# Kernel optimization log

Hardware: AMD Instinct MI355X
Metric: run time of the kernel (lower is better)

## Reference

```python
import jax, jax.numpy as jnp
import numpy as np

GAMMA = 0.00390625  # 1/256


def setup_inputs() -> dict:
    key = jax.random.key(0)
    ks = jax.random.split(key, 8)
    B, F, S = 65536, 256, 1024
    return {
        "x": jax.random.normal(ks[0], (B, F), dtype=jnp.float32),
        "sv": jax.random.normal(ks[1], (S, F), dtype=jnp.float32),
        "W1": jax.random.normal(ks[2], (S, S), dtype=jnp.float32) * (1.0 / np.sqrt(S)),
        "b1": jax.random.normal(ks[3], (S,), dtype=jnp.float32) * 0.01,
        "W2": jax.random.normal(ks[4], (S, S), dtype=jnp.float32) * (1.0 / np.sqrt(S)),
        "b2": jax.random.normal(ks[5], (S,), dtype=jnp.float32) * 0.01,
        "Wh": jax.random.normal(ks[6], (2, S), dtype=jnp.float32) * (1.0 / np.sqrt(S)),
        "bh": jax.random.normal(ks[7], (2,), dtype=jnp.float32) * 0.01,
    }


def reference(x, sv, W1, b1, W2, b2, Wh, bh):
    # RBF kernel features: k[b, s] = exp(-gamma * ||x_b - sv_s||^2)
    # Expand squared distance to avoid a (B, S, F) intermediate.
    x2 = jnp.sum(x * x, axis=-1, keepdims=True)          # (B, 1)
    s2 = jnp.sum(sv * sv, axis=-1)[None, :]              # (1, S)
    d2 = x2 + s2 - 2.0 * jnp.einsum("bf,sf->bs", x, sv)  # (B, S)
    k = jnp.exp(-GAMMA * d2)                              # (B, S)
    # MLP classifier: depth=2 hidden ReLU layers + 2-logit head
    h = jax.nn.relu(jnp.einsum("bs,os->bo", k, W1) + b1)
    h = jax.nn.relu(jnp.einsum("bs,os->bo", h, W2) + b2)
    return jnp.einsum("bs,os->bo", h, Wh) + bh           # (B, 2)
```

## Files before the change

kernel.cpp:

```cpp
#include <hip/hip_runtime.h>

typedef _Float16 f16x8 __attribute__((ext_vector_type(8)));
typedef _Float16 f16x4 __attribute__((ext_vector_type(4)));
typedef float    f32x4 __attribute__((ext_vector_type(4)));

#define GAMMA_F 0.00390625f

__global__ __launch_bounds__(256) void prep_rows_kernel(
    const float* __restrict__ src, _Float16* __restrict__ dst,
    float* __restrict__ sq, int nrows)
{
    int lane = threadIdx.x & 63, w = threadIdx.x >> 6;
    int row = blockIdx.x * 4 + w;
    if (row >= nrows) return;
    float4 v = ((const float4*)(src + (size_t)row * 256))[lane];
    f16x4 h;
    h[0] = (_Float16)v.x; h[1] = (_Float16)v.y;
    h[2] = (_Float16)v.z; h[3] = (_Float16)v.w;
    *((f16x4*)(dst + (size_t)row * 256) + lane) = h;
    float ss = v.x*v.x + v.y*v.y + v.z*v.z + v.w*v.w;
#pragma unroll
    for (int off = 32; off; off >>= 1) ss += __shfl_down(ss, off);
    if (lane == 0) sq[row] = ss;
}

__global__ __launch_bounds__(256) void cvt_kernel(
    const float* __restrict__ src, _Float16* __restrict__ dst, int n4)
{
    int i = blockIdx.x * 256 + threadIdx.x;
    if (i < n4) {
        float4 v = ((const float4*)src)[i];
        f16x4 h;
        h[0] = (_Float16)v.x; h[1] = (_Float16)v.y;
        h[2] = (_Float16)v.z; h[3] = (_Float16)v.w;
        ((f16x4*)dst)[i] = h;
    }
}

#define SBAR()  __builtin_amdgcn_s_barrier()
#define AS1 __attribute__((address_space(1)))
#define AS3 __attribute__((address_space(3)))

#define GLD(gptr, dstoff) __builtin_amdgcn_global_load_lds(                    \
    (const AS1 void*)(gptr), (AS3 void*)(ldsb + (dstoff)), 16, 0, 0)

#define STAGE_A(slot, half) do {                                               \
    GLD(aStage + (size_t)(half)*128*K,        (slot)*32768 + (half)*16384 + tb);          \
    GLD(aStage + (size_t)(half)*128*K + 64*K, (slot)*32768 + (half)*16384 + 8192 + tb);   \
} while (0)
#define STAGE_B(slot, half) do {                                               \
    GLD(bStage + (size_t)(half)*128*K,        65536 + (slot)*32768 + (half)*16384 + tb);        \
    GLD(bStage + (size_t)(half)*128*K + 64*K, 65536 + (slot)*32768 + (half)*16384 + 8192 + tb); \
} while (0)

#define READ_A(s, mh) do {                                                     \
    _Pragma("unroll") for (int mi = 0; mi < 4; ++mi) {                         \
        afr[0][mi] = *(const f16x8*)(ldsb + aO0 + (s)*32768 + (mh)*8192 + mi*2048); \
        afr[1][mi] = *(const f16x8*)(ldsb + aO1 + (s)*32768 + (mh)*8192 + mi*2048); \
    } } while (0)

#define READ_B(s, nh) do {                                                     \
    _Pragma("unroll") for (int nb = 0; nb < 2; ++nb) {                         \
        bfr[0][(nh)*2+nb] = *(const f16x8*)(ldsb + bO0 + (s)*32768 + (nh)*4096 + nb*2048); \
        bfr[1][(nh)*2+nb] = *(const f16x8*)(ldsb + bO1 + (s)*32768 + (nh)*4096 + nb*2048); \
    } } while (0)

#define MFMA16(mh, nh) do {                                                    \
    __builtin_amdgcn_s_setprio(1);                                             \
    _Pragma("unroll") for (int mi = 0; mi < 4; ++mi)                           \
    _Pragma("unroll") for (int nb = 0; nb < 2; ++nb)                           \
    _Pragma("unroll") for (int ks = 0; ks < 2; ++ks)                           \
        acc[(mh)*4+mi][(nh)*2+nb] = __builtin_amdgcn_mfma_f32_16x16x32_f16(    \
            afr[ks][mi], bfr[ks][(nh)*2+nb], acc[(mh)*4+mi][(nh)*2+nb], 0,0,0);\
    __builtin_amdgcn_s_setprio(0);                                             \
} while (0)

template <int MODE, int K>
__global__ __launch_bounds__(512, 1) void gemm256_kernel(
    const _Float16* __restrict__ A, const _Float16* __restrict__ B,
    _Float16* __restrict__ C, const float* __restrict__ e0,
    const float* __restrict__ e1)
{
    constexpr int KT = K / 64;
    constexpr int NITER = KT / 2;
    __shared__ f16x8 lds[8192];
    char* ldsb = (char*)lds;

    const int t    = threadIdx.x;
    const int tb   = t * 16;
    const int lane = t & 63, w = t >> 6;
    const int wr   = w >> 2, wc = w & 3;
    const int lrow = lane & 15, kq = lane >> 4;

    int bid  = blockIdx.x;
    int cpx  = (int)(gridDim.x >> 3);
    int lbid = (bid & 7) * cpx + (bid >> 3);
    int bm   = lbid >> 2, bn = lbid & 3;
    int rowA0 = bm * 256, rowB0 = bn * 256;

    const int aO0 = ((wr*128 + lrow)*8 + ( kq      ^ (lrow & 7))) * 16;
    const int aO1 = ((wr*128 + lrow)*8 + ((4 + kq) ^ (lrow & 7))) * 16;
    const int bO0 = 65536 + ((wc*64 + lrow)*8 + ( kq      ^ (lrow & 7))) * 16;
    const int bO1 = 65536 + ((wc*64 + lrow)*8 + ((4 + kq) ^ (lrow & 7))) * 16;

    const int prow = t >> 3;
    const int cg   = (t & 7) ^ (prow & 7);
    const _Float16* aStage = A + (size_t)(rowA0 + prow) * K + cg * 8;
    const _Float16* bStage = B + (size_t)(rowB0 + prow) * K + cg * 8;

    f32x4 acc[8][4];
#pragma unroll
    for (int i = 0; i < 8; ++i)
#pragma unroll
        for (int j = 0; j < 4; ++j) acc[i][j] = (f32x4){0.f, 0.f, 0.f, 0.f};

    f16x8 afr[2][4], bfr[2][4];

    STAGE_A(0, 0); STAGE_A(0, 1); STAGE_B(0, 0); STAGE_B(0, 1);
    aStage += 64; bStage += 64;
    STAGE_A(1, 0); STAGE_A(1, 1); STAGE_B(1, 0); STAGE_B(1, 1);
    aStage += 64; bStage += 64;
    asm volatile("s_waitcnt vmcnt(8)" ::: "memory");
    SBAR();

    for (int j = 0; j < NITER; ++j) {
        const bool last = (j == NITER - 1);

        READ_A(0, 0); READ_B(0, 0);
        if (j > 0) STAGE_A(1, 0);
        SBAR();
        MFMA16(0, 0);
        SBAR();
        READ_B(0, 1);
        if (j > 0) { STAGE_A(1, 1); aStage += 64; }
        SBAR();
        MFMA16(0, 1);
        SBAR();
        READ_A(0, 1);
        if (!last) STAGE_B(0, 0);
        SBAR();
        MFMA16(1, 0);
        SBAR();
        if (!last) {
            STAGE_B(0, 1); bStage += 64;
            asm volatile("s_waitcnt vmcnt(4)" ::: "memory");
        } else {
            asm volatile("s_waitcnt vmcnt(0)" ::: "memory");
        }
        SBAR();
        MFMA16(1, 1);
        SBAR();
        READ_A(1, 0); READ_B(1, 0);
        if (!last) STAGE_A(0, 0);
        SBAR();
        MFMA16(0, 0);
        SBAR();
        READ_B(1, 1);
        if (!last) { STAGE_A(0, 1); aStage += 64; }
        SBAR();
        MFMA16(0, 1);
        SBAR();
        READ_A(1, 1);
        if (!last) STAGE_B(1, 0);
        SBAR();
        MFMA16(1, 0);
        SBAR();
        if (!last) {
            STAGE_B(1, 1); bStage += 64;
            asm volatile("s_waitcnt vmcnt(4)" ::: "memory");
        }
        SBAR();
        MFMA16(1, 1);
        SBAR();
    }

    int gr0 = rowA0 + wr * 128;
    int gc0 = rowB0 + wc * 64;
    float ecol[4];
#pragma unroll
    for (int ni = 0; ni < 4; ++ni)
        ecol[ni] = (MODE == 0) ? e1[gc0 + ni * 16 + lrow]
                               : e0[gc0 + ni * 16 + lrow];
#pragma unroll
    for (int mi = 0; mi < 8; ++mi) {
#pragma unroll
        for (int jj = 0; jj < 4; ++jj) {
            int row = gr0 + mi * 16 + kq * 4 + jj;
            float xr = (MODE == 0) ? e0[row] : 0.f;
            size_t base = (size_t)row * 1024 + gc0 + lrow;
#pragma unroll
            for (int ni = 0; ni < 4; ++ni) {
                float v = acc[mi][ni][jj];
                if (MODE == 0) {
                    v = __expf(-GAMMA_F * (xr + ecol[ni] - 2.f * v));
                } else {
                    v += ecol[ni];
                    v = fmaxf(v, 0.f);
                }
                C[base + (size_t)ni * 16] = (_Float16)v;
            }
        }
    }
}

__global__ __launch_bounds__(256) void head_kernel(
    const _Float16* __restrict__ h2, const float* __restrict__ Wh,
    const float* __restrict__ bh, float* __restrict__ out)
{
    int lane = threadIdx.x & 63, w = threadIdx.x >> 6;
    int row = blockIdx.x * 4 + w;
    const _Float16* hp = h2 + (size_t)row * 1024;
    float s0 = 0.f, s1 = 0.f;
#pragma unroll
    for (int i = 0; i < 2; ++i) {
        int base = (i * 64 + lane) * 8;
        f16x8 hv = *(const f16x8*)(hp + base);
#pragma unroll
        for (int j = 0; j < 8; ++j) {
            float hj = (float)hv[j];
            s0 = fmaf(hj, Wh[base + j], s0);
            s1 = fmaf(hj, Wh[1024 + base + j], s1);
        }
    }
#pragma unroll
    for (int off = 32; off; off >>= 1) {
        s0 += __shfl_down(s0, off);
        s1 += __shfl_down(s1, off);
    }
    if (lane == 0) {
        out[(size_t)row * 2 + 0] = s0 + bh[0];
        out[(size_t)row * 2 + 1] = s1 + bh[1];
    }
}

extern "C" void kernel_launch(void* const* d_in, const int* in_sizes, int n_in,
                              void* d_out, int out_size, void* d_ws, size_t ws_size,
                              hipStream_t stream)
{
    const float* x  = (const float*)d_in[0];
    const float* sv = (const float*)d_in[1];
    const float* W1 = (const float*)d_in[2];
    const float* b1 = (const float*)d_in[3];
    const float* W2 = (const float*)d_in[4];
    const float* b2 = (const float*)d_in[5];
    const float* Wh = (const float*)d_in[6];
    const float* bh = (const float*)d_in[7];
    float* out = (float*)d_out;
    char* ws = (char*)d_ws;

    constexpr size_t OFF_SV = 0;
    constexpr size_t OFF_W1 = OFF_SV + 524288;
    constexpr size_t OFF_W2 = OFF_W1 + 2097152;
    constexpr size_t OFF_S2 = OFF_W2 + 2097152;
    constexpr size_t PERSIST = OFF_S2 + 4096;

    _Float16* svf = (_Float16*)(ws + OFF_SV);
    _Float16* w1f = (_Float16*)(ws + OFF_W1);
    _Float16* w2f = (_Float16*)(ws + OFF_W2);
    float*    s2v = (float*)(ws + OFF_S2);

    int Bc = 65536;
    while (Bc > 256 && PERSIST + (size_t)Bc * 4100ULL > ws_size) Bc >>= 1;

    char* chunk_base = ws + PERSIST;
    _Float16* kb  = (_Float16*)chunk_base;
    _Float16* h1b = (_Float16*)(chunk_base + (size_t)Bc * 2048);
    _Float16* xf  = h1b;
    float*    x2v = (float*)(chunk_base + (size_t)Bc * 4096);

    prep_rows_kernel<<<1024 / 4, 256, 0, stream>>>(sv, svf, s2v, 1024);
    cvt_kernel<<<1024, 256, 0, stream>>>(W1, w1f, 262144);
    cvt_kernel<<<1024, 256, 0, stream>>>(W2, w2f, 262144);

    int nchunks = 65536 / Bc;
    int ggrid   = (Bc / 256) * 4;
    for (int c = 0; c < nchunks; ++c) {
        const float* xc = x + (size_t)c * Bc * 256;
        prep_rows_kernel<<<Bc / 4, 256, 0, stream>>>(xc, xf, x2v, Bc);
        gemm256_kernel<0, 256><<<ggrid, 512, 0, stream>>>(xf, svf, kb, x2v, s2v);
        gemm256_kernel<1, 1024><<<ggrid, 512, 0, stream>>>(kb, w1f, h1b, b1, nullptr);
        gemm256_kernel<1, 1024><<<ggrid, 512, 0, stream>>>(h1b, w2f, kb, b2, nullptr);
        head_kernel<<<Bc / 4, 256, 0, stream>>>(kb, Wh, bh, out + (size_t)c * Bc * 2);
    }
}
```

Measured before the change: 398.0 us.

## Fuse output head into second hidden GEMM epilogue with atomics

The second hidden-layer GEMM now applies bias and ReLU and dots the result with both head weight rows in its epilogue. Partial sums are reduced across lanes and added to the output with atomics, which removes the separate head kernel and the f16 write and read of the second hidden activation. An init kernel seeds the output with the head bias. The MFMA loop order and LDS read/stage placement within the main loop are also reordered. In exchange, float atomic accumulation makes the output order-dependent and non-deterministic, and adds atomic traffic on a small output.

```diff
diff --git a/kernel.cpp b/kernel.cpp
--- a/kernel.cpp
+++ b/kernel.cpp
@@ -37,6 +37,13 @@
     }
 }
 
+__global__ __launch_bounds__(256) void init_out_kernel(
+    const float* __restrict__ bh, float* __restrict__ out, int n)
+{
+    int i = blockIdx.x * 256 + threadIdx.x;
+    if (i < n) ((float2*)out)[i] = make_float2(bh[0], bh[1]);
+}
+
 #define SBAR()  __builtin_amdgcn_s_barrier()
 #define AS1 __attribute__((address_space(1)))
 #define AS3 __attribute__((address_space(3)))
@@ -67,9 +74,9 @@
 
 #define MFMA16(mh, nh) do {                                                    \
     __builtin_amdgcn_s_setprio(1);                                             \
+    _Pragma("unroll") for (int ks = 0; ks < 2; ++ks)                           \
     _Pragma("unroll") for (int mi = 0; mi < 4; ++mi)                           \
     _Pragma("unroll") for (int nb = 0; nb < 2; ++nb)                           \
-    _Pragma("unroll") for (int ks = 0; ks < 2; ++ks)                           \
         acc[(mh)*4+mi][(nh)*2+nb] = __builtin_amdgcn_mfma_f32_16x16x32_f16(    \
             afr[ks][mi], bfr[ks][(nh)*2+nb], acc[(mh)*4+mi][(nh)*2+nb], 0,0,0);\
     __builtin_amdgcn_s_setprio(0);                                             \
@@ -79,7 +86,7 @@
 __global__ __launch_bounds__(512, 1) void gemm256_kernel(
     const _Float16* __restrict__ A, const _Float16* __restrict__ B,
     _Float16* __restrict__ C, const float* __restrict__ e0,
-    const float* __restrict__ e1)
+    const float* __restrict__ e1, float* __restrict__ outp)
 {
     constexpr int KT = K / 64;
     constexpr int NITER = KT / 2;
@@ -126,9 +133,10 @@
     for (int j = 0; j < NITER; ++j) {
         const bool last = (j == NITER - 1);
 
-        READ_A(0, 0); READ_B(0, 0);
+        READ_B(0, 0);
         if (j > 0) STAGE_A(1, 0);
         SBAR();
+        READ_A(0, 0);
         MFMA16(0, 0);
         SBAR();
         READ_B(0, 1);
@@ -136,9 +144,9 @@
         SBAR();
         MFMA16(0, 1);
         SBAR();
+        if (!last) STAGE_B(0, 0);
+        SBAR();
         READ_A(0, 1);
-        if (!last) STAGE_B(0, 0);
-        SBAR();
         MFMA16(1, 0);
         SBAR();
         if (!last) {
@@ -150,9 +158,10 @@
         SBAR();
         MFMA16(1, 1);
         SBAR();
-        READ_A(1, 0); READ_B(1, 0);
+        READ_B(1, 0);
         if (!last) STAGE_A(0, 0);
         SBAR();
+        READ_A(1, 0);
         MFMA16(0, 0);
         SBAR();
         READ_B(1, 1);
@@ -160,9 +169,9 @@
         SBAR();
         MFMA16(0, 1);
         SBAR();
+        if (!last) STAGE_B(1, 0);
+        SBAR();
         READ_A(1, 1);
-        if (!last) STAGE_B(1, 0);
-        SBAR();
         MFMA16(1, 0);
         SBAR();
         if (!last) {
@@ -181,6 +190,41 @@
     for (int ni = 0; ni < 4; ++ni)
         ecol[ni] = (MODE == 0) ? e1[gc0 + ni * 16 + lrow]
                                : e0[gc0 + ni * 16 + lrow];
+
+    if (MODE == 2) {
+        float wh0[4], wh1[4];
+#pragma unroll
+        for (int ni = 0; ni < 4; ++ni) {
+            int col = gc0 + ni * 16 + lrow;
+            wh0[ni] = e1[col];
+            wh1[ni] = e1[1024 + col];
+        }
+#pragma unroll
+        for (int mi = 0; mi < 8; ++mi) {
+#pragma unroll
+            for (int jj = 0; jj < 4; ++jj) {
+                int row = gr0 + mi * 16 + kq * 4 + jj;
+                float p0 = 0.f, p1 = 0.f;
+#pragma unroll
+                for (int ni = 0; ni < 4; ++ni) {
+                    float v = fmaxf(acc[mi][ni][jj] + ecol[ni], 0.f);
+                    p0 = fmaf(v, wh0[ni], p0);
+                    p1 = fmaf(v, wh1[ni], p1);
+                }
+#pragma unroll
+                for (int off = 1; off < 16; off <<= 1) {
+                    p0 += __shfl_xor(p0, off);
+                    p1 += __shfl_xor(p1, off);
+                }
+                if (lrow == 0) {
+                    atomicAdd(outp + (size_t)row * 2 + 0, p0);
+                    atomicAdd(outp + (size_t)row * 2 + 1, p1);
+                }
+            }
+        }
+        return;
+    }
+
 #pragma unroll
     for (int mi = 0; mi < 8; ++mi) {
 #pragma unroll
@@ -203,36 +247,6 @@
     }
 }
 
-__global__ __launch_bounds__(256) void head_kernel(
-    const _Float16* __restrict__ h2, const float* __restrict__ Wh,
-    const float* __restrict__ bh, float* __restrict__ out)
-{
-    int lane = threadIdx.x & 63, w = threadIdx.x >> 6;
-    int row = blockIdx.x * 4 + w;
-    const _Float16* hp = h2 + (size_t)row * 1024;
-    float s0 = 0.f, s1 = 0.f;
-#pragma unroll
-    for (int i = 0; i < 2; ++i) {
-        int base = (i * 64 + lane) * 8;
-        f16x8 hv = *(const f16x8*)(hp + base);
-#pragma unroll
-        for (int j = 0; j < 8; ++j) {
-            float hj = (float)hv[j];
-            s0 = fmaf(hj, Wh[base + j], s0);
-            s1 = fmaf(hj, Wh[1024 + base + j], s1);
-        }
-    }
-#pragma unroll
-    for (int off = 32; off; off >>= 1) {
-        s0 += __shfl_down(s0, off);
-        s1 += __shfl_down(s1, off);
-    }
-    if (lane == 0) {
-        out[(size_t)row * 2 + 0] = s0 + bh[0];
-        out[(size_t)row * 2 + 1] = s1 + bh[1];
-    }
-}
-
 extern "C" void kernel_launch(void* const* d_in, const int* in_sizes, int n_in,
                               void* d_out, int out_size, void* d_ws, size_t ws_size,
                               hipStream_t stream)
@@ -251,7 +265,8 @@
     constexpr size_t OFF_SV = 0;
     constexpr size_t OFF_W1 = OFF_SV + 524288;
     constexpr size_t OFF_W2 = OFF_W1 + 2097152;
-    constexpr size_t OFF_S2 = OFF_W2 + 2097152;
+    constexpr size_t OFF_WH = OFF_W2 + 2097152;
+    constexpr size_t OFF_S2 = OFF_WH + 8192;
     constexpr size_t PERSIST = OFF_S2 + 4096;
 
     _Float16* svf = (_Float16*)(ws + OFF_SV);
@@ -271,15 +286,16 @@
     prep_rows_kernel<<<1024 / 4, 256, 0, stream>>>(sv, svf, s2v, 1024);
     cvt_kernel<<<1024, 256, 0, stream>>>(W1, w1f, 262144);
     cvt_kernel<<<1024, 256, 0, stream>>>(W2, w2f, 262144);
+    init_out_kernel<<<256, 256, 0, stream>>>(bh, out, 65536);
 
     int nchunks = 65536 / Bc;
     int ggrid   = (Bc / 256) * 4;
     for (int c = 0; c < nchunks; ++c) {
         const float* xc = x + (size_t)c * Bc * 256;
         prep_rows_kernel<<<Bc / 4, 256, 0, stream>>>(xc, xf, x2v, Bc);
-        gemm256_kernel<0, 256><<<ggrid, 512, 0, stream>>>(xf, svf, kb, x2v, s2v);
-        gemm256_kernel<1, 1024><<<ggrid, 512, 0, stream>>>(kb, w1f, h1b, b1, nullptr);
-        gemm256_kernel<1, 1024><<<ggrid, 512, 0, stream>>>(h1b, w2f, kb, b2, nullptr);
-        head_kernel<<<Bc / 4, 256, 0, stream>>>(kb, Wh, bh, out + (size_t)c * Bc * 2);
-    }
-}
+        gemm256_kernel<0, 256><<<ggrid, 512, 0, stream>>>(xf, svf, kb, x2v, s2v, nullptr);
+        gemm256_kernel<1, 1024><<<ggrid, 512, 0, stream>>>(kb, w1f, h1b, b1, nullptr, nullptr);
+        gemm256_kernel<2, 1024><<<ggrid, 512, 0, stream>>>(h1b, w2f, kb, b2, Wh,
+                                                           out + (size_t)c * Bc * 2);
+    }
+}
```

After: 456.6 us. 1.15x slower.
